# Kernel optimization log

Hardware: AMD Instinct MI355X
Metric: run time of the kernel (lower is better)

The kernel has to match this reference:

```python
import jax, jax.numpy as jnp
import numpy as np

B, S, D, H, HD = 1, 2048, 1024, 16, 64
WINDOW = 512
RADIUS = max(1, WINDOW // 2)
GLOBAL_IDX = (0, 1, 2, 3)
NEG = -1e9


def rotate_half(x):
    x1, x2 = jnp.split(x, 2, axis=-1)
    return jnp.concatenate([-x2, x1], axis=-1)


def apply_rope(x, cos, sin, pos):
    # x: [b, s, h, hd]; cos/sin: [max_pos, hd]; pos: [b, s]
    c = cos[pos][:, :, None, :]
    s_ = sin[pos][:, :, None, :]
    return x * c + rotate_half(x) * s_


def setup_inputs() -> dict:
    key = jax.random.key(0)
    ks = jax.random.split(key, 12)
    x = jax.random.normal(ks[0], (B, S, D), dtype=jnp.float32)
    # RoPE tables (standard construction)
    inv_freq = 1.0 / (10000.0 ** (jnp.arange(0, HD, 2, dtype=jnp.float32) / HD))
    t = jnp.arange(S, dtype=jnp.float32)
    freqs = jnp.outer(t, inv_freq)                      # [S, HD/2]
    emb = jnp.concatenate([freqs, freqs], axis=-1)      # [S, HD]
    cos_freqs = jnp.cos(emb)
    sin_freqs = jnp.sin(emb)
    position_ids = jnp.broadcast_to(jnp.arange(S, dtype=jnp.int32), (B, S))
    w = lambda k: jax.random.normal(k, (D, D), dtype=jnp.float32) * 0.02
    return {
        "x": x, "cos_freqs": cos_freqs, "sin_freqs": sin_freqs,
        "position_ids": position_ids,
        "Wqs": w(ks[1]), "Wks": w(ks[2]), "Wvs": w(ks[3]),
        "Wqg": w(ks[4]), "Wkg": w(ks[5]), "Wvg": w(ks[6]),
        "Wo": w(ks[7]),
    }


def reference(x, cos_freqs, sin_freqs, position_ids, Wqs, Wks, Wvs, Wqg, Wkg, Wvg, Wo):
    b, s, d = x.shape
    split = lambda y: y.reshape(b, s, H, HD)
    qs = split(x @ Wqs)
    ks_ = split(x @ Wks)
    vs = split(x @ Wvs)
    kg = split(x @ Wkg)
    vg = split(x @ Wvg)
    # (qg projection exists in the module but is unused by its forward math)
    qs = apply_rope(qs, cos_freqs, sin_freqs, position_ids)
    ks_ = apply_rope(ks_, cos_freqs, sin_freqs, position_ids)

    qs_t = jnp.swapaxes(qs, 1, 2)   # [b,h,s,hd]
    ks_t = jnp.swapaxes(ks_, 1, 2)
    vs_t = jnp.swapaxes(vs, 1, 2)
    scale = 1.0 / jnp.sqrt(jnp.float32(HD))

    # local sliding-window (causal) attention over dense scores
    scores = jnp.einsum('bhsd,bhtd->bhst', qs_t, ks_t) * scale
    i = jnp.arange(s)[:, None]
    j = jnp.arange(s)[None, :]
    mask = (jnp.abs(i - j) <= RADIUS) & (j <= i)
    scores = jnp.where(mask[None, None], scores, NEG)
    g = jnp.array(GLOBAL_IDX)
    scores = scores.at[:, :, :, g].add(1e9)  # same as per-index set(score+1e9)
    attn = jax.nn.softmax(scores, axis=-1)
    out_local = jnp.einsum('bhst,bhtd->bhsd', attn, vs_t)
    out_local = jnp.swapaxes(out_local, 1, 2).reshape(b, s, d)

    # global attention: all queries attend to the global-index columns of kg/vg
    kg_t = jnp.swapaxes(kg, 1, 2)
    vg_t = jnp.swapaxes(vg, 1, 2)
    scores_g = jnp.einsum('bhsd,bhtd->bhst', qs_t, kg_t) * scale
    col_mask = jnp.zeros((s,), dtype=bool).at[g].set(True)
    scores_g = jnp.where(col_mask[None, None, None, :], scores_g, NEG)
    attn_g = jax.nn.softmax(scores_g, axis=-1)
    out_global = jnp.einsum('bhst,bhtd->bhsd', attn_g, vg_t)
    out_global = jnp.swapaxes(out_global, 1, 2).reshape(b, s, d)

    return (out_local + out_global) @ Wo
```

## Files before the change

kernel.cpp:

```cpp
#include <hip/hip_runtime.h>

typedef _Float16 half8 __attribute__((ext_vector_type(8)));
typedef float floatx4 __attribute__((ext_vector_type(4)));

#define SEQ 2048
#define DMODEL 1024
#define NHEADS 16
#define HEADDIM 64
#define PW 5120

__global__ __launch_bounds__(256) void k_prep(
    const float* __restrict__ x,
    const float* __restrict__ w0, const float* __restrict__ w1, const float* __restrict__ w2,
    const float* __restrict__ w3, const float* __restrict__ w4, const float* __restrict__ w5,
    _Float16* __restrict__ xh, _Float16* __restrict__ wcat, _Float16* __restrict__ wot) {
  const int tid = threadIdx.x;
  const int b = blockIdx.x;
  if (b < 1024) {
    int base = b * 2048 + tid * 8;
    floatx4 f0 = *(const floatx4*)(x + base);
    floatx4 f1 = *(const floatx4*)(x + base + 4);
    half8 h;
    #pragma unroll
    for (int e = 0; e < 4; ++e) { h[e] = (_Float16)f0[e]; h[e + 4] = (_Float16)f1[e]; }
    *(half8*)(xh + base) = h;
    return;
  }
  __shared__ _Float16 T[64][72];
  int t = b - 1024;
  int z = t >> 8;
  int tile = t & 255;
  int k0 = (tile >> 4) * 64, n0 = (tile & 15) * 64;
  const float* W = (z == 0) ? w0 : (z == 1) ? w1 : (z == 2) ? w2
                 : (z == 3) ? w3 : (z == 4) ? w4 : w5;
  _Float16* dst = (z < 5) ? (wcat + (size_t)z * 1024 * 1024) : wot;

  int lr = tid >> 2, c0 = (tid & 3) * 16;
  #pragma unroll
  for (int i = 0; i < 4; ++i) {
    floatx4 f = *(const floatx4*)(W + (size_t)(k0 + lr) * DMODEL + n0 + c0 + i * 4);
    #pragma unroll
    for (int e = 0; e < 4; ++e) T[c0 + i * 4 + e][lr] = (_Float16)f[e];
  }
  __syncthreads();
  int nr = tid >> 2, s0 = (tid & 3) * 16;
  #pragma unroll
  for (int i = 0; i < 2; ++i) {
    half8 h = *(const half8*)&T[nr][s0 + i * 8];
    *(half8*)(dst + (size_t)(n0 + nr) * DMODEL + k0 + s0 + i * 8) = h;
  }
}

template <bool HALF_OUT, bool FUSE_ROPE, bool SPARSE>
__global__ __launch_bounds__(256, 2) void k_gemm128b(
    const _Float16* __restrict__ A, const _Float16* __restrict__ Bt,
    void* __restrict__ Cv, float* __restrict__ Cp0, float* __restrict__ Cp1,
    const float* __restrict__ cos_t, const float* __restrict__ sin_t,
    const int* __restrict__ pos, int M, int N, int K, int kLen) {
  __shared__ _Float16 As[128][128];
  __shared__ _Float16 Bs[128][128];
  const int tid = threadIdx.x;
  const int lane = tid & 63;
  const int w = tid >> 6;
  const int wm = (w >> 1) * 64;
  const int wn = (w & 1) * 64;
  const int l15 = lane & 15;
  const int q4 = lane >> 4;
  int m0, n0, kStart;
  if (SPARSE) {
    int b = blockIdx.x;
    if (b < 384) { m0 = (b & 15) * 128; n0 = (b >> 4) * 128; }
    else         { m0 = 0;              n0 = 3072 + (b - 384) * 128; }
    kStart = 0;
  } else {
    m0 = blockIdx.x * 128;
    n0 = blockIdx.y * 128;
    kStart = blockIdx.z * kLen;
  }

  floatx4 acc[4][4];
  #pragma unroll
  for (int i = 0; i < 4; ++i)
    #pragma unroll
    for (int j = 0; j < 4; ++j) acc[i][j] = (floatx4){0.f, 0.f, 0.f, 0.f};

  _Float16* asBase = &As[0][0];
  _Float16* bsBase = &Bs[0][0];
  const int swz = l15 & 7;

  for (int k0 = kStart; k0 < kStart + kLen; k0 += 128) {
    __syncthreads();
    #pragma unroll
    for (int it = 0; it < 8; ++it) {
      int c = it * 256 + tid;
      int r = c >> 4, cc = c & 15;
      int g = cc ^ (r & 7);
      __builtin_amdgcn_global_load_lds(
          (const __attribute__((address_space(1))) void*)(A + (size_t)(m0 + r) * K + k0 + g * 8),
          (__attribute__((address_space(3))) void*)(asBase + (it * 256 + w * 64) * 8),
          16, 0, 0);
      __builtin_amdgcn_global_load_lds(
          (const __attribute__((address_space(1))) void*)(Bt + (size_t)(n0 + r) * K + k0 + g * 8),
          (__attribute__((address_space(3))) void*)(bsBase + (it * 256 + w * 64) * 8),
          16, 0, 0);
    }
    __syncthreads();

    #pragma unroll
    for (int kk = 0; kk < 4; ++kk) {
      int q = kk * 4 + q4;
      half8 af[4], bf[4];
      #pragma unroll
      for (int t = 0; t < 4; ++t) {
        int ar = wm + t * 16 + l15;
        af[t] = *(const half8*)(asBase + (size_t)ar * 128 + ((q ^ swz) * 8));
        int br = wn + t * 16 + l15;
        bf[t] = *(const half8*)(bsBase + (size_t)br * 128 + ((q ^ swz) * 8));
      }
      #pragma unroll
      for (int i = 0; i < 4; ++i)
        #pragma unroll
        for (int j = 0; j < 4; ++j)
          acc[i][j] = __builtin_amdgcn_mfma_f32_16x16x32_f16(af[i], bf[j], acc[i][j], 0, 0, 0);
    }
  }

  float* P = HALF_OUT ? nullptr : ((!SPARSE && blockIdx.z) ? Cp1 : Cp0);
  #pragma unroll
  for (int tm = 0; tm < 4; ++tm) {
    #pragma unroll
    for (int r = 0; r < 4; ++r) {
      int row = m0 + wm + tm * 16 + q4 * 4 + r;
      float v[4];
      #pragma unroll
      for (int tn = 0; tn < 4; ++tn) v[tn] = acc[tm][tn][r];
      if (FUSE_ROPE && n0 < 2048) {
        int p = pos[row];
        #pragma unroll
        for (int tn = 0; tn < 2; ++tn) {
          int d = tn * 16 + l15;
          float a = acc[tm][tn][r];
          float bvv = acc[tm][tn + 2][r];
          float c1 = cos_t[p * 64 + d],      s1 = sin_t[p * 64 + d];
          float c2 = cos_t[p * 64 + d + 32], s2 = sin_t[p * 64 + d + 32];
          v[tn]     = a * c1 - bvv * s1;
          v[tn + 2] = bvv * c2 + a * s2;
        }
      }
      #pragma unroll
      for (int tn = 0; tn < 4; ++tn) {
        int col = n0 + wn + tn * 16 + l15;
        if (HALF_OUT)
          ((_Float16*)Cv)[(size_t)row * N + col] = (_Float16)v[tn];
        else
          P[(size_t)row * N + col] = v[tn];
      }
    }
  }
}

__global__ __launch_bounds__(256) void k_reduce(const float* __restrict__ p0,
                                                const float* __restrict__ p1,
                                                float* __restrict__ out) {
  int i = (blockIdx.x * 256 + threadIdx.x) * 4;
  floatx4 a = *(const floatx4*)(p0 + i);
  floatx4 b = *(const floatx4*)(p1 + i);
  *(floatx4*)(out + i) = a + b;
}

__global__ __launch_bounds__(256, 2) void k_attn(const _Float16* __restrict__ proj,
                                                 _Float16* __restrict__ out) {
  const int tid = threadIdx.x;
  const int hb = blockIdx.y * 64;

  if (blockIdx.x >= 14) {
    const int i = (blockIdx.x - 14) * 4 + (tid >> 6);
    const int lane = tid & 63;
    const float scale = 0.125f;
    float qv = (float)proj[(size_t)i * PW + hb + lane];
    float sg[4];
    #pragma unroll
    for (int g = 0; g < 4; ++g) {
      float kgv = (float)proj[(size_t)g * PW + 3072 + hb + lane];
      float v = qv * kgv;
      #pragma unroll
      for (int off = 32; off; off >>= 1) v += __shfl_xor(v, off, 64);
      sg[g] = v * scale;
    }
    float mg = fmaxf(fmaxf(sg[0], sg[1]), fmaxf(sg[2], sg[3]));
    float dg = 0.f, og = 0.f;
    #pragma unroll
    for (int g = 0; g < 4; ++g) {
      float p = __expf(sg[g] - mg);
      dg += p;
      og += p * (float)proj[(size_t)g * PW + 4096 + hb + lane];
    }
    og /= dg;
    int jmin = (i >= 256) ? (i - 256) : 0;
    int jmax = (i < 3) ? i : 3;
    float acc = 0.f;
    for (int j = jmin; j <= jmax; ++j)
      acc += (float)proj[(size_t)j * PW + 2048 + hb + lane];
    float ol = acc / (float)(jmax - jmin + 1);
    out[(size_t)i * DMODEL + hb + lane] = (_Float16)(ol + og);
    return;
  }

  const int i0 = 256 + blockIdx.x * 128;
  const int jlo = i0 - 256;
  const int lane = tid & 63;
  const int w = tid >> 6;
  const int l15 = lane & 15;
  const int q4 = lane >> 4;

  __shared__ _Float16 Qs[128][72];
  __shared__ _Float16 Kc[64][72];
  __shared__ _Float16 Vtc[64][72];
  __shared__ _Float16 Ps[128][72];
  __shared__ _Float16 kg_s[4][64];
  __shared__ _Float16 vg_s[4][64];
  __shared__ float svg_s[64];
  __shared__ float pg_s[4][128];

  #pragma unroll
  for (int rep = 0; rep < 4; ++rep) {
    int c = tid + rep * 256;
    int r = c >> 3, q = c & 7;
    *(half8*)&Qs[r][q * 8] = *(const half8*)(proj + (size_t)(i0 + r) * PW + hb + q * 8);
  }
  {
    int g = tid >> 6, c2 = tid & 63;
    kg_s[g][c2] = proj[(size_t)g * PW + 3072 + hb + c2];
    vg_s[g][c2] = proj[(size_t)g * PW + 4096 + hb + c2];
    if (tid < 64) {
      float s = 0.f;
      #pragma unroll
      for (int g2 = 0; g2 < 4; ++g2) s += (float)proj[(size_t)g2 * PW + 2048 + hb + tid];
      svg_s[tid] = s;
    }
  }
  __syncthreads();

  #pragma unroll
  for (int pass = 0; pass < 2; ++pass) {
    int ro = pass * 64 + w * 16 + (lane >> 2);
    int part = lane & 3;
    float sg[4];
    #pragma unroll
    for (int g = 0; g < 4; ++g) {
      float acc = 0.f;
      #pragma unroll
      for (int u = 0; u < 16; ++u)
        acc += (float)Qs[ro][part * 16 + u] * (float)kg_s[g][part * 16 + u];
      acc += __shfl_xor(acc, 1, 64);
      acc += __shfl_xor(acc, 2, 64);
      sg[g] = acc * 0.125f;
    }
    float mg = fmaxf(fmaxf(sg[0], sg[1]), fmaxf(sg[2], sg[3]));
    float dg = 0.f;
    #pragma unroll
    for (int g = 0; g < 4; ++g) dg += __expf(sg[g] - mg);
    pg_s[part][ro] = __expf(sg[part] - mg) / dg;
  }

  half8 qf[2][2];
  #pragma unroll
  for (int rg = 0; rg < 2; ++rg) {
    int row = w * 32 + rg * 16 + l15;
    qf[rg][0] = *(const half8*)&Qs[row][q4 * 8];
    qf[rg][1] = *(const half8*)&Qs[row][32 + q4 * 8];
  }

  float lpart[2][4];
  floatx4 oacc[2][4];
  #pragma unroll
  for (int rg = 0; rg < 2; ++rg)
    #pragma unroll
    for (int cb = 0; cb < 4; ++cb) {
      oacc[rg][cb] = (floatx4){0.f, 0.f, 0.f, 0.f};
      lpart[rg][cb] = 0.f;
    }

  for (int cc = 0; cc < 6; ++cc) {
    const int jbase = jlo + cc * 64;
    __syncthreads();
    #pragma unroll
    for (int rep = 0; rep < 2; ++rep) {
      int c = tid + rep * 256;
      int r = c >> 3, q = c & 7;
      *(half8*)&Kc[r][q * 8] =
          *(const half8*)(proj + (size_t)(jbase + r) * PW + 1024 + hb + q * 8);
    }
    #pragma unroll
    for (int it = 0; it < 2; ++it) {
      int idx = it * 256 + tid;
      int j = (idx & 7) + ((idx >> 6) << 3);
      int d0 = ((idx >> 3) & 7) * 8;
      half8 vv = *(const half8*)(proj + (size_t)(jbase + j) * PW + 2048 + hb + d0);
      #pragma unroll
      for (int u = 0; u < 8; ++u) Vtc[d0 + u][j] = vv[u];
    }
    __syncthreads();

    #pragma unroll
    for (int rg = 0; rg < 2; ++rg) {
      float sc[4][4];
      #pragma unroll
      for (int cb = 0; cb < 4; ++cb) {
        half8 b0 = *(const half8*)&Kc[cb * 16 + l15][q4 * 8];
        half8 b1 = *(const half8*)&Kc[cb * 16 + l15][32 + q4 * 8];
        floatx4 a = (floatx4){0.f, 0.f, 0.f, 0.f};
        a = __builtin_amdgcn_mfma_f32_16x16x32_f16(qf[rg][0], b0, a, 0, 0, 0);
        a = __builtin_amdgcn_mfma_f32_16x16x32_f16(qf[rg][1], b1, a, 0, 0, 0);
        #pragma unroll
        for (int r = 0; r < 4; ++r) sc[cb][r] = a[r];
      }

      #pragma unroll
      for (int r = 0; r < 4; ++r) {
        int ri = w * 32 + rg * 16 + q4 * 4 + r;
        float rowp = 0.f;
        #pragma unroll
        for (int cb = 0; cb < 4; ++cb) {
          int jjg = cc * 64 + cb * 16 + l15;
          bool valid = (jjg >= ri) && (jjg <= ri + 256);
          float p = valid ? __expf(sc[cb][r] * 0.125f) : 0.f;
          Ps[ri][cb * 16 + l15] = (_Float16)p;
          rowp += p;
        }
        lpart[rg][r] += rowp;
      }

      half8 pf0 = *(const half8*)&Ps[w * 32 + rg * 16 + l15][q4 * 8];
      half8 pf1 = *(const half8*)&Ps[w * 32 + rg * 16 + l15][32 + q4 * 8];
      #pragma unroll
      for (int cb = 0; cb < 4; ++cb) {
        half8 v0 = *(const half8*)&Vtc[cb * 16 + l15][q4 * 8];
        half8 v1 = *(const half8*)&Vtc[cb * 16 + l15][32 + q4 * 8];
        oacc[rg][cb] = __builtin_amdgcn_mfma_f32_16x16x32_f16(pf0, v0, oacc[rg][cb], 0, 0, 0);
        oacc[rg][cb] = __builtin_amdgcn_mfma_f32_16x16x32_f16(pf1, v1, oacc[rg][cb], 0, 0, 0);
      }
    }
  }

  #pragma unroll
  for (int rg = 0; rg < 2; ++rg)
    #pragma unroll
    for (int r = 0; r < 4; ++r) {
      int ri = w * 32 + rg * 16 + q4 * 4 + r;
      if (i0 + ri < 260) continue;
      float lsum = lpart[rg][r];
      #pragma unroll
      for (int off = 1; off < 16; off <<= 1) lsum += __shfl_xor(lsum, off, 64);
      float inv = 1.f / (lsum + 4.f);
      #pragma unroll
      for (int cb = 0; cb < 4; ++cb) {
        int col = cb * 16 + l15;
        float ol = (oacc[rg][cb][r] + svg_s[col]) * inv;
        float og = 0.f;
        #pragma unroll
        for (int g = 0; g < 4; ++g) og += pg_s[g][ri] * (float)vg_s[g][col];
        out[(size_t)(i0 + ri) * DMODEL + hb + col] = (_Float16)(ol + og);
      }
    }
}

extern "C" void kernel_launch(void* const* d_in, const int* in_sizes, int n_in,
                              void* d_out, int out_size, void* d_ws, size_t ws_size,
                              hipStream_t stream) {
  const float* x     = (const float*)d_in[0];
  const float* cos_t = (const float*)d_in[1];
  const float* sin_t = (const float*)d_in[2];
  const int*   pos   = (const int*)d_in[3];
  const float* Wqs   = (const float*)d_in[4];
  const float* Wks   = (const float*)d_in[5];
  const float* Wvs   = (const float*)d_in[6];
  const float* Wkg   = (const float*)d_in[8];
  const float* Wvg   = (const float*)d_in[9];
  const float* Wo    = (const float*)d_in[10];
  float* out = (float*)d_out;

  char* ws = (char*)d_ws;
  _Float16* xh   = (_Float16*)(ws);
  _Float16* wcat = (_Float16*)(ws + (4u << 20));
  _Float16* wot  = (_Float16*)(ws + (14u << 20));
  _Float16* proj = (_Float16*)(ws + (16u << 20));
  _Float16* attn = (_Float16*)(ws + (36u << 20));
  float* p0 = (float*)(ws);
  float* p1 = (float*)(ws + (16u << 20));

  k_prep<<<2560, 256, 0, stream>>>(x, Wqs, Wks, Wvs, Wkg, Wvg, Wo, xh, wcat, wot);
  k_gemm128b<true, true, true><<<400, 256, 0, stream>>>(
      xh, wcat, proj, nullptr, nullptr, cos_t, sin_t, pos, SEQ, PW, DMODEL, DMODEL);
  k_attn<<<dim3(79, NHEADS), 256, 0, stream>>>(proj, attn);
  k_gemm128b<false, false, false><<<dim3(16, 8, 2), 256, 0, stream>>>(
      attn, wot, nullptr, p0, p1, cos_t, sin_t, pos, SEQ, DMODEL, DMODEL, 512);
  k_reduce<<<SEQ * DMODEL / 1024, 256, 0, stream>>>(p0, p1, out);
}
```

Before: 164.8 us.

## Halve attention query tile, prefetch K/V into registers, swizzle transposed V tile

The attention kernel now processes 64 query rows per block instead of 128. That cuts the key window to 5 chunks instead of 6, so less wasted out-of-window work per query, and the grid grows to 93 blocks per head for more parallelism. The next K/V chunk is loaded into registers while the current chunk is being computed, which overlaps global loads with MFMA work. The transposed V shared tile uses an XOR swizzle to reduce LDS bank conflicts on its scattered stores. The trade-off is that Q loads and global-score setup are amortized over fewer rows, and each block does less MFMA work per synchronization.

```diff
diff --git a/kernel.cpp b/kernel.cpp
--- a/kernel.cpp
+++ b/kernel.cpp
@@ -173,8 +173,8 @@
   const int tid = threadIdx.x;
   const int hb = blockIdx.y * 64;
 
-  if (blockIdx.x >= 14) {
-    const int i = (blockIdx.x - 14) * 4 + (tid >> 6);
+  if (blockIdx.x >= 28) {
+    const int i = (blockIdx.x - 28) * 4 + (tid >> 6);
     const int lane = tid & 63;
     const float scale = 0.125f;
     float qv = (float)proj[(size_t)i * PW + hb + lane];
@@ -206,24 +206,24 @@
     return;
   }
 
-  const int i0 = 256 + blockIdx.x * 128;
+  const int i0 = 256 + blockIdx.x * 64;
   const int jlo = i0 - 256;
   const int lane = tid & 63;
   const int w = tid >> 6;
   const int l15 = lane & 15;
   const int q4 = lane >> 4;
 
-  __shared__ _Float16 Qs[128][72];
+  __shared__ _Float16 Qs[64][72];
   __shared__ _Float16 Kc[64][72];
   __shared__ _Float16 Vtc[64][72];
-  __shared__ _Float16 Ps[128][72];
+  __shared__ _Float16 Ps[64][72];
   __shared__ _Float16 kg_s[4][64];
   __shared__ _Float16 vg_s[4][64];
   __shared__ float svg_s[64];
-  __shared__ float pg_s[4][128];
-
-  #pragma unroll
-  for (int rep = 0; rep < 4; ++rep) {
+  __shared__ float pg_s[4][64];
+
+  #pragma unroll
+  for (int rep = 0; rep < 2; ++rep) {
     int c = tid + rep * 256;
     int r = c >> 3, q = c & 7;
     *(half8*)&Qs[r][q * 8] = *(const half8*)(proj + (size_t)(i0 + r) * PW + hb + q * 8);
@@ -241,9 +241,8 @@
   }
   __syncthreads();
 
-  #pragma unroll
-  for (int pass = 0; pass < 2; ++pass) {
-    int ro = pass * 64 + w * 16 + (lane >> 2);
+  {
+    int ro = w * 16 + (lane >> 2);
     int part = lane & 3;
     float sg[4];
     #pragma unroll
@@ -263,106 +262,110 @@
     pg_s[part][ro] = __expf(sg[part] - mg) / dg;
   }
 
-  half8 qf[2][2];
-  #pragma unroll
-  for (int rg = 0; rg < 2; ++rg) {
-    int row = w * 32 + rg * 16 + l15;
-    qf[rg][0] = *(const half8*)&Qs[row][q4 * 8];
-    qf[rg][1] = *(const half8*)&Qs[row][32 + q4 * 8];
-  }
-
-  float lpart[2][4];
-  floatx4 oacc[2][4];
-  #pragma unroll
-  for (int rg = 0; rg < 2; ++rg)
+  half8 qf0 = *(const half8*)&Qs[w * 16 + l15][q4 * 8];
+  half8 qf1 = *(const half8*)&Qs[w * 16 + l15][32 + q4 * 8];
+
+  float lpart[4];
+  floatx4 oacc[4];
+  #pragma unroll
+  for (int cb = 0; cb < 4; ++cb) {
+    oacc[cb] = (floatx4){0.f, 0.f, 0.f, 0.f};
+    lpart[cb] = 0.f;
+  }
+
+  const int kr_r0 = tid >> 3, kr_q = tid & 7;
+  const int kr_r1 = kr_r0 + 32;
+  const int vj0 = (tid & 7) + ((tid >> 6) << 3);
+  const int vj1 = vj0 + 32;
+  const int vd0 = ((tid >> 3) & 7) * 8;
+
+  half8 kr0, kr1, vr0, vr1;
+  {
+    const _Float16* kb = proj + (size_t)jlo * PW + 1024 + hb;
+    const _Float16* vb = proj + (size_t)jlo * PW + 2048 + hb;
+    kr0 = *(const half8*)(kb + (size_t)kr_r0 * PW + kr_q * 8);
+    kr1 = *(const half8*)(kb + (size_t)kr_r1 * PW + kr_q * 8);
+    vr0 = *(const half8*)(vb + (size_t)vj0 * PW + vd0);
+    vr1 = *(const half8*)(vb + (size_t)vj1 * PW + vd0);
+  }
+
+  for (int cc = 0; cc < 5; ++cc) {
+    __syncthreads();
+    *(half8*)&Kc[kr_r0][kr_q * 8] = kr0;
+    *(half8*)&Kc[kr_r1][kr_q * 8] = kr1;
+    #pragma unroll
+    for (int u = 0; u < 8; ++u) {
+      int d = vd0 + u;
+      Vtc[d][vj0 ^ (d & 56)] = vr0[u];
+      Vtc[d][vj1 ^ (d & 56)] = vr1[u];
+    }
+    if (cc < 4) {
+      const _Float16* kb = proj + (size_t)(jlo + (cc + 1) * 64) * PW + 1024 + hb;
+      const _Float16* vb = proj + (size_t)(jlo + (cc + 1) * 64) * PW + 2048 + hb;
+      kr0 = *(const half8*)(kb + (size_t)kr_r0 * PW + kr_q * 8);
+      kr1 = *(const half8*)(kb + (size_t)kr_r1 * PW + kr_q * 8);
+      vr0 = *(const half8*)(vb + (size_t)vj0 * PW + vd0);
+      vr1 = *(const half8*)(vb + (size_t)vj1 * PW + vd0);
+    }
+    __syncthreads();
+
+    float sc[4][4];
     #pragma unroll
     for (int cb = 0; cb < 4; ++cb) {
-      oacc[rg][cb] = (floatx4){0.f, 0.f, 0.f, 0.f};
-      lpart[rg][cb] = 0.f;
-    }
-
-  for (int cc = 0; cc < 6; ++cc) {
-    const int jbase = jlo + cc * 64;
-    __syncthreads();
-    #pragma unroll
-    for (int rep = 0; rep < 2; ++rep) {
-      int c = tid + rep * 256;
-      int r = c >> 3, q = c & 7;
-      *(half8*)&Kc[r][q * 8] =
-          *(const half8*)(proj + (size_t)(jbase + r) * PW + 1024 + hb + q * 8);
-    }
-    #pragma unroll
-    for (int it = 0; it < 2; ++it) {
-      int idx = it * 256 + tid;
-      int j = (idx & 7) + ((idx >> 6) << 3);
-      int d0 = ((idx >> 3) & 7) * 8;
-      half8 vv = *(const half8*)(proj + (size_t)(jbase + j) * PW + 2048 + hb + d0);
-      #pragma unroll
-      for (int u = 0; u < 8; ++u) Vtc[d0 + u][j] = vv[u];
-    }
-    __syncthreads();
-
-    #pragma unroll
-    for (int rg = 0; rg < 2; ++rg) {
-      float sc[4][4];
+      half8 b0 = *(const half8*)&Kc[cb * 16 + l15][q4 * 8];
+      half8 b1 = *(const half8*)&Kc[cb * 16 + l15][32 + q4 * 8];
+      floatx4 a = (floatx4){0.f, 0.f, 0.f, 0.f};
+      a = __builtin_amdgcn_mfma_f32_16x16x32_f16(qf0, b0, a, 0, 0, 0);
+      a = __builtin_amdgcn_mfma_f32_16x16x32_f16(qf1, b1, a, 0, 0, 0);
+      #pragma unroll
+      for (int r = 0; r < 4; ++r) sc[cb][r] = a[r];
+    }
+
+    #pragma unroll
+    for (int r = 0; r < 4; ++r) {
+      int ri = w * 16 + q4 * 4 + r;
+      float rowp = 0.f;
       #pragma unroll
       for (int cb = 0; cb < 4; ++cb) {
-        half8 b0 = *(const half8*)&Kc[cb * 16 + l15][q4 * 8];
-        half8 b1 = *(const half8*)&Kc[cb * 16 + l15][32 + q4 * 8];
-        floatx4 a = (floatx4){0.f, 0.f, 0.f, 0.f};
-        a = __builtin_amdgcn_mfma_f32_16x16x32_f16(qf[rg][0], b0, a, 0, 0, 0);
-        a = __builtin_amdgcn_mfma_f32_16x16x32_f16(qf[rg][1], b1, a, 0, 0, 0);
-        #pragma unroll
-        for (int r = 0; r < 4; ++r) sc[cb][r] = a[r];
+        int jjg = cc * 64 + cb * 16 + l15;
+        bool valid = (jjg >= ri) && (jjg <= ri + 256);
+        float p = valid ? __expf(sc[cb][r] * 0.125f) : 0.f;
+        Ps[ri][cb * 16 + l15] = (_Float16)p;
+        rowp += p;
       }
-
-      #pragma unroll
-      for (int r = 0; r < 4; ++r) {
-        int ri = w * 32 + rg * 16 + q4 * 4 + r;
-        float rowp = 0.f;
-        #pragma unroll
-        for (int cb = 0; cb < 4; ++cb) {
-          int jjg = cc * 64 + cb * 16 + l15;
-          bool valid = (jjg >= ri) && (jjg <= ri + 256);
-          float p = valid ? __expf(sc[cb][r] * 0.125f) : 0.f;
-          Ps[ri][cb * 16 + l15] = (_Float16)p;
-          rowp += p;
-        }
-        lpart[rg][r] += rowp;
-      }
-
-      half8 pf0 = *(const half8*)&Ps[w * 32 + rg * 16 + l15][q4 * 8];
-      half8 pf1 = *(const half8*)&Ps[w * 32 + rg * 16 + l15][32 + q4 * 8];
-      #pragma unroll
-      for (int cb = 0; cb < 4; ++cb) {
-        half8 v0 = *(const half8*)&Vtc[cb * 16 + l15][q4 * 8];
-        half8 v1 = *(const half8*)&Vtc[cb * 16 + l15][32 + q4 * 8];
-        oacc[rg][cb] = __builtin_amdgcn_mfma_f32_16x16x32_f16(pf0, v0, oacc[rg][cb], 0, 0, 0);
-        oacc[rg][cb] = __builtin_amdgcn_mfma_f32_16x16x32_f16(pf1, v1, oacc[rg][cb], 0, 0, 0);
-      }
-    }
-  }
-
-  #pragma unroll
-  for (int rg = 0; rg < 2; ++rg)
-    #pragma unroll
-    for (int r = 0; r < 4; ++r) {
-      int ri = w * 32 + rg * 16 + q4 * 4 + r;
-      if (i0 + ri < 260) continue;
-      float lsum = lpart[rg][r];
-      #pragma unroll
-      for (int off = 1; off < 16; off <<= 1) lsum += __shfl_xor(lsum, off, 64);
-      float inv = 1.f / (lsum + 4.f);
-      #pragma unroll
-      for (int cb = 0; cb < 4; ++cb) {
-        int col = cb * 16 + l15;
-        float ol = (oacc[rg][cb][r] + svg_s[col]) * inv;
-        float og = 0.f;
-        #pragma unroll
-        for (int g = 0; g < 4; ++g) og += pg_s[g][ri] * (float)vg_s[g][col];
-        out[(size_t)(i0 + ri) * DMODEL + hb + col] = (_Float16)(ol + og);
-      }
-    }
+      lpart[r] += rowp;
+    }
+
+    half8 pf0 = *(const half8*)&Ps[w * 16 + l15][q4 * 8];
+    half8 pf1 = *(const half8*)&Ps[w * 16 + l15][32 + q4 * 8];
+    #pragma unroll
+    for (int cb = 0; cb < 4; ++cb) {
+      int dv = cb * 16 + l15;
+      half8 v0 = *(const half8*)&Vtc[dv][(q4 * 8) ^ (dv & 56)];
+      half8 v1 = *(const half8*)&Vtc[dv][(32 + q4 * 8) ^ (dv & 56)];
+      oacc[cb] = __builtin_amdgcn_mfma_f32_16x16x32_f16(pf0, v0, oacc[cb], 0, 0, 0);
+      oacc[cb] = __builtin_amdgcn_mfma_f32_16x16x32_f16(pf1, v1, oacc[cb], 0, 0, 0);
+    }
+  }
+
+  #pragma unroll
+  for (int r = 0; r < 4; ++r) {
+    int ri = w * 16 + q4 * 4 + r;
+    if (i0 + ri < 260) continue;
+    float lsum = lpart[r];
+    #pragma unroll
+    for (int off = 1; off < 16; off <<= 1) lsum += __shfl_xor(lsum, off, 64);
+    float inv = 1.f / (lsum + 4.f);
+    #pragma unroll
+    for (int cb = 0; cb < 4; ++cb) {
+      int col = cb * 16 + l15;
+      float ol = (oacc[cb][r] + svg_s[col]) * inv;
+      float og = 0.f;
+      #pragma unroll
+      for (int g = 0; g < 4; ++g) og += pg_s[g][ri] * (float)vg_s[g][col];
+      out[(size_t)(i0 + ri) * DMODEL + hb + col] = (_Float16)(ol + og);
+    }
+  }
 }
 
 extern "C" void kernel_launch(void* const* d_in, const int* in_sizes, int n_in,
@@ -392,7 +395,7 @@
   k_prep<<<2560, 256, 0, stream>>>(x, Wqs, Wks, Wvs, Wkg, Wvg, Wo, xh, wcat, wot);
   k_gemm128b<true, true, true><<<400, 256, 0, stream>>>(
       xh, wcat, proj, nullptr, nullptr, cos_t, sin_t, pos, SEQ, PW, DMODEL, DMODEL);
-  k_attn<<<dim3(79, NHEADS), 256, 0, stream>>>(proj, attn);
+  k_attn<<<dim3(93, NHEADS), 256, 0, stream>>>(proj, attn);
   k_gemm128b<false, false, false><<<dim3(16, 8, 2), 256, 0, stream>>>(
       attn, wot, nullptr, p0, p1, cos_t, sin_t, pos, SEQ, DMODEL, DMODEL, 512);
   k_reduce<<<SEQ * DMODEL / 1024, 256, 0, stream>>>(p0, p1, out);
```

After: 160.5 us. 2.6% less time.
